# Kernel tuning notes

Hardware: AMD Instinct MI355X
Metric: run time of the kernel (lower is better)

Reference implementation:

```python
import jax, jax.numpy as jnp
import numpy as np
from jax import lax

B, H, W, C = 32, 64, 64, 192
DIN = 2 * C  # expand=2
EPS = 1e-5


def setup_inputs() -> dict:
    key = jax.random.key(0)
    ks = jax.random.split(key, 12)
    s = 0.02
    return {
        "x": jax.random.normal(ks[0], (B, H, W, C), dtype=jnp.float32),
        "norm_w": jnp.ones((C,), jnp.float32),
        "norm_b": jnp.zeros((C,), jnp.float32),
        "sel_w1": jax.random.normal(ks[1], (16, 4), jnp.float32) * 0.5,
        "sel_b1": jnp.zeros((16,), jnp.float32),
        "sel_w2": jax.random.normal(ks[2], (4, 16), jnp.float32) * 0.5,
        "sel_b2": jnp.zeros((4,), jnp.float32),
        "fc1_w": jax.random.normal(ks[3], (DIN, C), jnp.float32) * s,
        "fc1_b": jnp.zeros((DIN,), jnp.float32),
        "conv_w": jax.random.normal(ks[4], (DIN, 1, 3), jnp.float32) * 0.3,
        "conv_b": jnp.zeros((DIN,), jnp.float32),
        "fc2_w": jax.random.normal(ks[5], (C, DIN), jnp.float32) * s,
        "fc2_b": jnp.zeros((C,), jnp.float32),
    }


def _scan_dir(x, d):
    # x: [B,H,W,C] -> [B,L,C]; dirs = ['h','v','d','a'] (v and d are identical)
    b, h, w, c = x.shape
    if d == 0:  # 'h'
        return x.reshape(b, h * w, c)
    if d in (1, 2):  # 'v' / 'd': transpose then flatten
        return x.transpose(0, 2, 1, 3).reshape(b, w * h, c)
    # 'a': flip W, transpose, flatten
    return jnp.flip(x, axis=2).transpose(0, 2, 1, 3).reshape(b, w * h, c)


def _seq_block(s, fc1_w, fc1_b, conv_w, conv_b, fc2_w, fc2_b):
    # s: [B,L,C]
    h = jnp.einsum('blc,dc->bld', s, fc1_w) + fc1_b  # [B,L,DIN]
    hc = h.transpose(0, 2, 1)  # [B,DIN,L]
    hc = lax.conv_general_dilated(
        hc, conv_w, window_strides=(1,), padding=[(1, 1)],
        dimension_numbers=('NCH', 'OIH', 'NCH'),
        feature_group_count=conv_w.shape[0])
    hc = hc + conv_b[None, :, None]
    h = jax.nn.gelu(hc.transpose(0, 2, 1), approximate=False)
    return jnp.einsum('bld,cd->blc', h, fc2_w) + fc2_b


def reference(x, norm_w, norm_b, sel_w1, sel_b1, sel_w2, sel_b2,
              fc1_w, fc1_b, conv_w, conv_b, fc2_w, fc2_b):
    b, h, w, c = x.shape
    # LayerNorm over channels
    mu = x.mean(-1, keepdims=True)
    var = ((x - mu) ** 2).mean(-1, keepdims=True)
    xn = (x - mu) / jnp.sqrt(var + EPS) * norm_w + norm_b

    # Gradient-based direction selector
    g = xn.mean(-1)[:, None]  # [B,1,H,W]
    gp = jnp.pad(g, ((0, 0), (0, 0), (1, 1), (1, 1)), mode='reflect')
    grad_h = jnp.abs(gp[:, :, :, 2:] - gp[:, :, :, :-2])  # [B,1,H+2,W]
    grad_v = jnp.abs(gp[:, :, 2:, :] - gp[:, :, :-2, :])  # [B,1,H,W+2]
    sh = grad_h.mean(axis=(2, 3))  # [B,1]
    sv = grad_v.mean(axis=(2, 3))
    scores = jnp.concatenate([sh, sv, (sh + sv) / 2, jnp.abs(sh - sv)], axis=1)
    hid = jax.nn.relu(scores @ sel_w1.T + sel_b1)
    logits = hid @ sel_w2.T + sel_b2  # [B,4]
    dir_idx = jnp.argmax(logits, axis=-1)  # topk=1 -> argmax of softmax

    # Compute all 4 direction branches batched, then per-sample select
    outs = []
    for d in range(4):
        seq = _scan_dir(xn, d)
        proc = _seq_block(seq, fc1_w, fc1_b, conv_w, conv_b, fc2_w, fc2_b)
        outs.append(proc.reshape(b, h, w, c))  # unscan = plain reshape (as in source)
    stacked = jnp.stack(outs)  # [4,B,H,W,C]
    sel = stacked[dir_idx, jnp.arange(b)]  # [B,H,W,C]
    return x + sel
```

## Files before the change

kernel.cpp:

```cpp
#include <hip/hip_runtime.h>
#include <hip/hip_bf16.h>
#include <math.h>


typedef __bf16 bf16x8 __attribute__((ext_vector_type(8)));
typedef float f32x4 __attribute__((ext_vector_type(4)));
typedef __hip_bfloat16 hb;

#define XN_OFF   0
#define G_OFF    50331648
#define W1S_OFF  50855936
#define W2S_OFF  51003392
#define DIR_OFF  51150848

__device__ __forceinline__ float fast_gelu(float v) {
  float u = v * (0.7978845608f + 0.0356774081f * v * v);
  float a = fabsf(u);
  float e = __expf(-2.f * a);
  float tt = (1.f - e) * __builtin_amdgcn_rcpf(1.f + e);
  tt = copysignf(tt, u);
  return 0.5f * v * (1.f + tt);
}

__device__ __forceinline__ unsigned short bf16bits(float f) {
  hb h = __float2bfloat16(f);
  return *reinterpret_cast<unsigned short*>(&h);
}

__global__ __launch_bounds__(256) void ln_kernel(
    const float* __restrict__ x, const float* __restrict__ nw,
    const float* __restrict__ nb, hb* __restrict__ xn, float* __restrict__ g) {
  __shared__ float4 xt[768];
  __shared__ unsigned int ytu[1536];
  __shared__ float snw[192], snb[192];
  int t = threadIdx.x;
  long pixbase = (long)blockIdx.x * 16;
  const float4* x4 = (const float4*)(x + pixbase * 192);
  #pragma unroll
  for (int i = 0; i < 3; i++) xt[t + i * 256] = x4[t + i * 256];
  if (t < 192) { snw[t] = nw[t]; snb[t] = nb[t]; }
  __syncthreads();

  int p = t >> 4, sub = t & 15;
  const float4* row = xt + p * 48 + sub * 3;
  float4 f0 = row[0], f1 = row[1], f2 = row[2];
  float v[12] = {f0.x, f0.y, f0.z, f0.w, f1.x, f1.y, f1.z, f1.w,
                 f2.x, f2.y, f2.z, f2.w};
  float s1 = 0.f, s2 = 0.f;
  #pragma unroll
  for (int i = 0; i < 12; i++) { s1 += v[i]; s2 += v[i] * v[i]; }
  #pragma unroll
  for (int off = 8; off; off >>= 1) {
    s1 += __shfl_xor(s1, off);
    s2 += __shfl_xor(s2, off);
  }
  float mu = s1 * (1.f / 192.f);
  float var = s2 * (1.f / 192.f) - mu * mu;
  float rstd = rsqrtf(var + 1e-5f);
  int c0 = sub * 12;
  float ys[12], gs = 0.f;
  #pragma unroll
  for (int i = 0; i < 12; i++) {
    ys[i] = (v[i] - mu) * rstd * snw[c0 + i] + snb[c0 + i];
    gs += ys[i];
  }
  #pragma unroll
  for (int off = 8; off; off >>= 1) gs += __shfl_xor(gs, off);
  if (sub == 0) g[pixbase + p] = gs * (1.f / 192.f);
  unsigned int* yo = ytu + p * 96 + sub * 6;
  #pragma unroll
  for (int i = 0; i < 6; i++)
    yo[i] = (unsigned int)bf16bits(ys[2 * i]) |
            ((unsigned int)bf16bits(ys[2 * i + 1]) << 16);
  __syncthreads();
  const float4* yt4 = (const float4*)ytu;
  float4* o4 = (float4*)(xn + pixbase * 192);
  o4[t] = yt4[t];
  if (t < 128) o4[t + 256] = yt4[t + 256];
}

__global__ __launch_bounds__(256) void sel_kernel(
    const float* __restrict__ g, const float* __restrict__ w1,
    const float* __restrict__ b1, const float* __restrict__ w2,
    const float* __restrict__ b2, int* __restrict__ dir) {
  __shared__ float gt[64][65];
  __shared__ float red[8];
  int b = blockIdx.x, t = threadIdx.x;
  const float* gb = g + (long)b * 4096;
  for (int i = t; i < 4096; i += 256) gt[i >> 6][i & 63] = gb[i];
  __syncthreads();
  float ah = 0.f, av = 0.f;
  for (int i = t; i < 3968; i += 256) {
    int r = i / 62, j = i - r * 62 + 1;
    float d = fabsf(gt[r][j + 1] - gt[r][j - 1]);
    if (r == 1 || r == 62) d *= 2.f;
    ah += d;
  }
  for (int i = t; i < 3968; i += 256) {
    int r = (i >> 6) + 1, c = i & 63;
    float d = fabsf(gt[r + 1][c] - gt[r - 1][c]);
    if (c == 1 || c == 62) d *= 2.f;
    av += d;
  }
  #pragma unroll
  for (int off = 32; off; off >>= 1) {
    ah += __shfl_xor(ah, off);
    av += __shfl_xor(av, off);
  }
  if ((t & 63) == 0) { red[(t >> 6) * 2] = ah; red[(t >> 6) * 2 + 1] = av; }
  __syncthreads();
  if (t == 0) {
    float sh = 0.f, sv = 0.f;
    for (int w = 0; w < 4; w++) { sh += red[w * 2]; sv += red[w * 2 + 1]; }
    sh *= (1.f / 4224.f);
    sv *= (1.f / 4224.f);
    float sc[4] = {sh, sv, 0.5f * (sh + sv), fabsf(sh - sv)};
    float hid[16];
    #pragma unroll
    for (int i = 0; i < 16; i++) {
      float a = b1[i];
      for (int k = 0; k < 4; k++) a += sc[k] * w1[i * 4 + k];
      hid[i] = fmaxf(a, 0.f);
    }
    float best = -1e30f; int bi = 0;
    for (int j = 0; j < 4; j++) {
      float a = b2[j];
      for (int i = 0; i < 16; i++) a += hid[i] * w2[j * 16 + i];
      if (a > best) { best = a; bi = j; }
    }
    dir[b] = bi;
  }
}

__global__ __launch_bounds__(256) void wshuf_kernel(
    const float* __restrict__ fc1_w, const float* __restrict__ fc2_w,
    hb* __restrict__ w1s, hb* __restrict__ w2s) {
  int idx = blockIdx.x * 256 + threadIdx.x;
  const float* w; hb* o; int K, KS, li;
  if (idx < 73728) { w = fc1_w; o = w1s; K = 192; KS = 6;  li = idx; }
  else             { w = fc2_w; o = w2s; K = 384; KS = 12; li = idx - 73728; }
  int j = li & 7, lane = (li >> 3) & 63, f = li >> 9;
  int ks = f % KS, nt = f / KS;
  int n = nt * 16 + (lane & 15);
  int k = ks * 32 + ((lane >> 4) << 3) + j;
  o[li] = __float2bfloat16(w[n * K + k]);
}

#define SH_STR 196
__global__ __launch_bounds__(256, 4) void fused_kernel(
    const hb* __restrict__ xn, const hb* __restrict__ w1s, const hb* __restrict__ w2s,
    const float* __restrict__ fc1_b, const float* __restrict__ fc2_b,
    const float* __restrict__ conv_w, const float* __restrict__ conv_b,
    const float* __restrict__ x, const int* __restrict__ dirp,
    float* __restrict__ out) {
  __shared__ hb sH[2][32 * SH_STR];
  __shared__ float4 cvt[384];
  __shared__ float sB1[384];
  __shared__ float sB2[192];

  int b = blockIdx.y, mt = blockIdx.x;
  int dir = dirp[b];
  int l0 = mt * 30;
  int t = threadIdx.x;

  for (int d = t; d < 384; d += 256) {
    cvt[d] = make_float4(conv_w[d * 3], conv_w[d * 3 + 1], conv_w[d * 3 + 2], conv_b[d]);
    sB1[d] = fc1_b[d];
  }
  if (t < 192) sB2[t] = fc2_b[t];

  int wave = t >> 6, lane = t & 63;
  int m16 = lane & 15, q = lane >> 4;
  const hb* xnb = xn + (long)b * 4096 * 192;

  bf16x8 af[2][6];
  #pragma unroll
  for (int tl = 0; tl < 2; tl++) {
    int hr = tl * 16 + m16;
    int l = l0 - 1 + hr;
    int lc = min(max(l, 0), 4095);
    int src;
    if (dir == 0)      src = lc;
    else if (dir == 3) src = ((lc & 63) << 6) + 63 - (lc >> 6);
    else               src = ((lc & 63) << 6) + (lc >> 6);
    const bf16x8* ap = (const bf16x8*)(xnb + (long)src * 192) + q;
    #pragma unroll
    for (int ks = 0; ks < 6; ks++) af[tl][ks] = ap[ks * 4];
  }
  __syncthreads();

  {
    int buf = wave >> 1;
    int ntbase = wave * 6;
    #pragma unroll
    for (int i = 0; i < 6; i++) {
      int nt = ntbase + i;
      const bf16x8* bp = (const bf16x8*)w1s + (long)(nt * 6) * 64 + lane;
      f32x4 c0 = {0.f, 0.f, 0.f, 0.f}, c1 = {0.f, 0.f, 0.f, 0.f};
      #pragma unroll
      for (int ks = 0; ks < 6; ks++) {
        bf16x8 bf = bp[ks * 64];
        c0 = __builtin_amdgcn_mfma_f32_16x16x32_bf16(af[0][ks], bf, c0, 0, 0, 0);
        c1 = __builtin_amdgcn_mfma_f32_16x16x32_bf16(af[1][ks], bf, c1, 0, 0, 0);
      }
      float bias = sB1[nt * 16 + m16];
      int ncol = (nt - buf * 12) * 16 + m16;
      hb* s = &sH[buf][0];
      #pragma unroll
      for (int r = 0; r < 4; r++) {
        s[(q * 4 + r) * SH_STR + ncol]      = __float2bfloat16(c0[r] + bias);
        s[(16 + q * 4 + r) * SH_STR + ncol] = __float2bfloat16(c1[r] + bias);
      }
    }
  }
  __syncthreads();

  int tile2 = wave & 1, nth = wave >> 1;
  int hr = tile2 * 16 + m16;
  int l_c = l0 - 1 + hr;
  bool hm_ok = (l_c >= 1);
  bool hp_ok = (l_c <= 4094);
  int rm = hr > 0 ? hr - 1 : 0;
  int rp = hr < 31 ? hr + 1 : 31;
  bf16x8 af2[12];
  #pragma unroll
  for (int ks = 0; ks < 12; ks++) {
    int bb = ks / 6, kl = ks - bb * 6;
    int col = kl * 32 + q * 8;
    const hb* base = &sH[bb][0];
    bf16x8 vm = *(const bf16x8*)(base + rm * SH_STR + col);
    bf16x8 vc = *(const bf16x8*)(base + hr * SH_STR + col);
    bf16x8 vp = *(const bf16x8*)(base + rp * SH_STR + col);
    int d0 = ks * 32 + q * 8;
    bf16x8 o;
    #pragma unroll
    for (int j = 0; j < 8; j++) {
      float4 cw = cvt[d0 + j];
      float hm = hm_ok ? (float)vm[j] : 0.f;
      float hc = (float)vc[j];
      float hp = hp_ok ? (float)vp[j] : 0.f;
      o[j] = (__bf16)fast_gelu(hm * cw.x + hc * cw.y + hp * cw.z + cw.w);
    }
    af2[ks] = o;
  }
  f32x4 acc[6];
  #pragma unroll
  for (int i = 0; i < 6; i++) acc[i] = (f32x4){0.f, 0.f, 0.f, 0.f};
  #pragma unroll
  for (int i2 = 0; i2 < 6; i2++) {
    int nt2 = nth * 6 + i2;
    const bf16x8* bp = (const bf16x8*)w2s + (long)(nt2 * 12) * 64 + lane;
    #pragma unroll
    for (int ks = 0; ks < 12; ks++)
      acc[i2] = __builtin_amdgcn_mfma_f32_16x16x32_bf16(af2[ks], bp[ks * 64], acc[i2], 0, 0, 0);
  }

  #pragma unroll
  for (int i2 = 0; i2 < 6; i2++) {
    int c = (nth * 6 + i2) * 16 + m16;
    float bias = sB2[c];
    #pragma unroll
    for (int r = 0; r < 4; r++) {
      int hr_r = tile2 * 16 + q * 4 + r;
      int l_r = l0 - 1 + hr_r;
      if (hr_r >= 1 && hr_r <= 30 && l_r <= 4095) {
        long idx = ((long)b * 4096 + l_r) * 192 + c;
        out[idx] = x[idx] + acc[i2][r] + bias;
      }
    }
  }
}

extern "C" void kernel_launch(void* const* d_in, const int* in_sizes, int n_in,
                              void* d_out, int out_size, void* d_ws, size_t ws_size,
                              hipStream_t stream) {
  const float* x      = (const float*)d_in[0];
  const float* norm_w = (const float*)d_in[1];
  const float* norm_b = (const float*)d_in[2];
  const float* sel_w1 = (const float*)d_in[3];
  const float* sel_b1 = (const float*)d_in[4];
  const float* sel_w2 = (const float*)d_in[5];
  const float* sel_b2 = (const float*)d_in[6];
  const float* fc1_w  = (const float*)d_in[7];
  const float* fc1_b  = (const float*)d_in[8];
  const float* conv_w = (const float*)d_in[9];
  const float* conv_b = (const float*)d_in[10];
  const float* fc2_w  = (const float*)d_in[11];
  const float* fc2_b  = (const float*)d_in[12];
  float* out = (float*)d_out;
  char* ws = (char*)d_ws;

  hb* xn    = (hb*)(ws + XN_OFF);
  float* g  = (float*)(ws + G_OFF);
  hb* w1s   = (hb*)(ws + W1S_OFF);
  hb* w2s   = (hb*)(ws + W2S_OFF);
  int* dir  = (int*)(ws + DIR_OFF);

  wshuf_kernel<<<576, 256, 0, stream>>>(fc1_w, fc2_w, w1s, w2s);
  ln_kernel<<<8192, 256, 0, stream>>>(x, norm_w, norm_b, xn, g);
  sel_kernel<<<32, 256, 0, stream>>>(g, sel_w1, sel_b1, sel_w2, sel_b2, dir);
  dim3 gg(137, 32);
  fused_kernel<<<gg, 256, 0, stream>>>(xn, w1s, w2s, fc1_b, fc2_b,
                                       conv_w, conv_b, x, dir, out);
}
```

Measured before the change: 357.6 us.

## Merge weight shuffle into LN kernel, interleave conv-GELU with fc2 MFMAs

Folds the weight-shuffle kernel into the layernorm launch as extra blocks, which saves one kernel launch. It simplifies the tanh-GELU to a single exp and reciprocal, and moves the fc1/fc2 biases from shared memory into registers. It also interleaves the conv+GELU computation for each k-slice directly with the fc2 MFMAs instead of buffering 12 A-fragments, and raises the occupancy hint to 5 blocks per CU. The risks are register pressure from the occupancy target and possible exp overflow in the new GELU form for large inputs, where 1+e becomes infinite (that case does resolve to v).

```diff
diff --git a/kernel.cpp b/kernel.cpp
--- a/kernel.cpp
+++ b/kernel.cpp
@@ -15,11 +15,9 @@
 
 __device__ __forceinline__ float fast_gelu(float v) {
   float u = v * (0.7978845608f + 0.0356774081f * v * v);
-  float a = fabsf(u);
-  float e = __expf(-2.f * a);
-  float tt = (1.f - e) * __builtin_amdgcn_rcpf(1.f + e);
-  tt = copysignf(tt, u);
-  return 0.5f * v * (1.f + tt);
+  float e = __expf(2.f * u);
+  float r = __builtin_amdgcn_rcpf(1.f + e);
+  return v - v * r;
 }
 
 __device__ __forceinline__ unsigned short bf16bits(float f) {
@@ -27,13 +25,27 @@
   return *reinterpret_cast<unsigned short*>(&h);
 }
 
-__global__ __launch_bounds__(256) void ln_kernel(
+__global__ __launch_bounds__(256) void ln_wshuf_kernel(
     const float* __restrict__ x, const float* __restrict__ nw,
-    const float* __restrict__ nb, hb* __restrict__ xn, float* __restrict__ g) {
+    const float* __restrict__ nb, hb* __restrict__ xn, float* __restrict__ g,
+    const float* __restrict__ fc1_w, const float* __restrict__ fc2_w,
+    hb* __restrict__ w1s, hb* __restrict__ w2s) {
+  int t = threadIdx.x;
+  if (blockIdx.x >= 8192) {
+    int idx = (blockIdx.x - 8192) * 256 + t;
+    const float* w; hb* o; int K, KS, li;
+    if (idx < 73728) { w = fc1_w; o = w1s; K = 192; KS = 6;  li = idx; }
+    else             { w = fc2_w; o = w2s; K = 384; KS = 12; li = idx - 73728; }
+    int j = li & 7, lane = (li >> 3) & 63, f = li >> 9;
+    int ks = f % KS, nt = f / KS;
+    int n = nt * 16 + (lane & 15);
+    int k = ks * 32 + ((lane >> 4) << 3) + j;
+    o[li] = __float2bfloat16(w[n * K + k]);
+    return;
+  }
   __shared__ float4 xt[768];
   __shared__ unsigned int ytu[1536];
   __shared__ float snw[192], snb[192];
-  int t = threadIdx.x;
   long pixbase = (long)blockIdx.x * 16;
   const float4* x4 = (const float4*)(x + pixbase * 192);
   #pragma unroll
@@ -132,22 +144,8 @@
   }
 }
 
-__global__ __launch_bounds__(256) void wshuf_kernel(
-    const float* __restrict__ fc1_w, const float* __restrict__ fc2_w,
-    hb* __restrict__ w1s, hb* __restrict__ w2s) {
-  int idx = blockIdx.x * 256 + threadIdx.x;
-  const float* w; hb* o; int K, KS, li;
-  if (idx < 73728) { w = fc1_w; o = w1s; K = 192; KS = 6;  li = idx; }
-  else             { w = fc2_w; o = w2s; K = 384; KS = 12; li = idx - 73728; }
-  int j = li & 7, lane = (li >> 3) & 63, f = li >> 9;
-  int ks = f % KS, nt = f / KS;
-  int n = nt * 16 + (lane & 15);
-  int k = ks * 32 + ((lane >> 4) << 3) + j;
-  o[li] = __float2bfloat16(w[n * K + k]);
-}
-
 #define SH_STR 196
-__global__ __launch_bounds__(256, 4) void fused_kernel(
+__global__ __launch_bounds__(256, 5) void fused_kernel(
     const hb* __restrict__ xn, const hb* __restrict__ w1s, const hb* __restrict__ w2s,
     const float* __restrict__ fc1_b, const float* __restrict__ fc2_b,
     const float* __restrict__ conv_w, const float* __restrict__ conv_b,
@@ -155,23 +153,25 @@
     float* __restrict__ out) {
   __shared__ hb sH[2][32 * SH_STR];
   __shared__ float4 cvt[384];
-  __shared__ float sB1[384];
-  __shared__ float sB2[192];
 
   int b = blockIdx.y, mt = blockIdx.x;
   int dir = dirp[b];
   int l0 = mt * 30;
   int t = threadIdx.x;
 
-  for (int d = t; d < 384; d += 256) {
+  for (int d = t; d < 384; d += 256)
     cvt[d] = make_float4(conv_w[d * 3], conv_w[d * 3 + 1], conv_w[d * 3 + 2], conv_b[d]);
-    sB1[d] = fc1_b[d];
-  }
-  if (t < 192) sB2[t] = fc2_b[t];
 
   int wave = t >> 6, lane = t & 63;
   int m16 = lane & 15, q = lane >> 4;
+  int tile2 = wave & 1, nth = wave >> 1;
   const hb* xnb = xn + (long)b * 4096 * 192;
+
+  float b1r[6], b2r[6];
+  #pragma unroll
+  for (int i = 0; i < 6; i++) b1r[i] = fc1_b[(wave * 6 + i) * 16 + m16];
+  #pragma unroll
+  for (int i = 0; i < 6; i++) b2r[i] = fc2_b[(nth * 6 + i) * 16 + m16];
 
   bf16x8 af[2][6];
   #pragma unroll
@@ -203,7 +203,7 @@
         c0 = __builtin_amdgcn_mfma_f32_16x16x32_bf16(af[0][ks], bf, c0, 0, 0, 0);
         c1 = __builtin_amdgcn_mfma_f32_16x16x32_bf16(af[1][ks], bf, c1, 0, 0, 0);
       }
-      float bias = sB1[nt * 16 + m16];
+      float bias = b1r[i];
       int ncol = (nt - buf * 12) * 16 + m16;
       hb* s = &sH[buf][0];
       #pragma unroll
@@ -215,14 +215,19 @@
   }
   __syncthreads();
 
-  int tile2 = wave & 1, nth = wave >> 1;
   int hr = tile2 * 16 + m16;
   int l_c = l0 - 1 + hr;
   bool hm_ok = (l_c >= 1);
   bool hp_ok = (l_c <= 4094);
   int rm = hr > 0 ? hr - 1 : 0;
   int rp = hr < 31 ? hr + 1 : 31;
-  bf16x8 af2[12];
+  const bf16x8* bp2 = (const bf16x8*)w2s + (long)(nth * 6) * 12 * 64 + lane;
+
+  f32x4 acc[6];
+  #pragma unroll
+  for (int i = 0; i < 6; i++) acc[i] = (f32x4){0.f, 0.f, 0.f, 0.f};
+
+  bf16x8 z8 = {};
   #pragma unroll
   for (int ks = 0; ks < 12; ks++) {
     int bb = ks / 6, kl = ks - bb * 6;
@@ -231,34 +236,27 @@
     bf16x8 vm = *(const bf16x8*)(base + rm * SH_STR + col);
     bf16x8 vc = *(const bf16x8*)(base + hr * SH_STR + col);
     bf16x8 vp = *(const bf16x8*)(base + rp * SH_STR + col);
+    if (!hm_ok) vm = z8;
+    if (!hp_ok) vp = z8;
     int d0 = ks * 32 + q * 8;
-    bf16x8 o;
+    bf16x8 a;
     #pragma unroll
     for (int j = 0; j < 8; j++) {
       float4 cw = cvt[d0 + j];
-      float hm = hm_ok ? (float)vm[j] : 0.f;
-      float hc = (float)vc[j];
-      float hp = hp_ok ? (float)vp[j] : 0.f;
-      o[j] = (__bf16)fast_gelu(hm * cw.x + hc * cw.y + hp * cw.z + cw.w);
-    }
-    af2[ks] = o;
-  }
-  f32x4 acc[6];
-  #pragma unroll
-  for (int i = 0; i < 6; i++) acc[i] = (f32x4){0.f, 0.f, 0.f, 0.f};
-  #pragma unroll
-  for (int i2 = 0; i2 < 6; i2++) {
-    int nt2 = nth * 6 + i2;
-    const bf16x8* bp = (const bf16x8*)w2s + (long)(nt2 * 12) * 64 + lane;
-    #pragma unroll
-    for (int ks = 0; ks < 12; ks++)
-      acc[i2] = __builtin_amdgcn_mfma_f32_16x16x32_bf16(af2[ks], bp[ks * 64], acc[i2], 0, 0, 0);
+      float s = fmaf((float)vm[j], cw.x,
+                fmaf((float)vc[j], cw.y,
+                fmaf((float)vp[j], cw.z, cw.w)));
+      a[j] = (__bf16)fast_gelu(s);
+    }
+    #pragma unroll
+    for (int i2 = 0; i2 < 6; i2++)
+      acc[i2] = __builtin_amdgcn_mfma_f32_16x16x32_bf16(a, bp2[(i2 * 12 + ks) * 64], acc[i2], 0, 0, 0);
   }
 
   #pragma unroll
   for (int i2 = 0; i2 < 6; i2++) {
     int c = (nth * 6 + i2) * 16 + m16;
-    float bias = sB2[c];
+    float bias = b2r[i2];
     #pragma unroll
     for (int r = 0; r < 4; r++) {
       int hr_r = tile2 * 16 + q * 4 + r;
@@ -296,8 +294,8 @@
   hb* w2s   = (hb*)(ws + W2S_OFF);
   int* dir  = (int*)(ws + DIR_OFF);
 
-  wshuf_kernel<<<576, 256, 0, stream>>>(fc1_w, fc2_w, w1s, w2s);
-  ln_kernel<<<8192, 256, 0, stream>>>(x, norm_w, norm_b, xn, g);
+  ln_wshuf_kernel<<<8768, 256, 0, stream>>>(x, norm_w, norm_b, xn, g,
+                                            fc1_w, fc2_w, w1s, w2s);
   sel_kernel<<<32, 256, 0, stream>>>(g, sel_w1, sel_b1, sel_w2, sel_b2, dir);
   dim3 gg(137, 32);
   fused_kernel<<<gg, 256, 0, stream>>>(xn, w1s, w2s, fc1_b, fc2_b,
```

Result: slower. 403.6 us (+12.9%).
